# Performance work log

Measured on AMD Instinct MI355X. Metric: run time of the kernel, lower is better.

Reference implementation:

```python
import jax, jax.numpy as jnp
import numpy as np

N_NODES = 40000
N_EDGES = 640000
IN_CH = 128
OUT_CH = 128
BN_EPS = 1e-5


def setup_inputs() -> dict:
    key = jax.random.key(0)
    ks = jax.random.split(key, 8)
    x = jax.random.normal(ks[0], (N_NODES, IN_CH), dtype=jnp.float32)
    edge_index = jax.random.randint(ks[1], (2, N_EDGES), 0, N_NODES, dtype=jnp.int64)
    s1 = 1.0 / np.sqrt(IN_CH)
    s2 = 1.0 / np.sqrt(OUT_CH)
    W1 = jax.random.uniform(ks[2], (OUT_CH, IN_CH), jnp.float32, -s1, s1)
    b1 = jax.random.uniform(ks[3], (OUT_CH,), jnp.float32, -s1, s1)
    gamma = jnp.ones((OUT_CH,), jnp.float32)
    beta = jnp.zeros((OUT_CH,), jnp.float32)
    W2 = jax.random.uniform(ks[4], (OUT_CH, OUT_CH), jnp.float32, -s2, s2)
    b2 = jax.random.uniform(ks[5], (OUT_CH,), jnp.float32, -s2, s2)
    eps = jnp.float32(0.0)
    return {"x": x, "edge_index": edge_index, "W1": W1, "b1": b1,
            "gamma": gamma, "beta": beta, "W2": W2, "b2": b2, "eps": eps}


def reference(x, edge_index, W1, b1, gamma, beta, W2, b2, eps):
    src, dst = edge_index[0], edge_index[1]
    # neighbor sum: agg[v] = sum_{(u,v) in E} x[u]
    agg = jax.ops.segment_sum(x[src], dst, num_segments=N_NODES)  # [N, in_ch]
    h = (1.0 + eps) * x + agg
    # Linear 1
    h = h @ W1.T + b1  # [N, out_ch]
    # BatchNorm1d (training mode: batch stats, biased variance)
    mu = jnp.mean(h, axis=0)
    var = jnp.var(h, axis=0)
    h = (h - mu) * jax.lax.rsqrt(var + BN_EPS) * gamma + beta
    # ReLU + Linear 2
    h = jnp.maximum(h, 0.0)
    return h @ W2.T + b2
```

## Files before the change

### kernel.cpp

```cpp
#include <hip/hip_runtime.h>

#define NN 40000
#define NE 640000
#define BN_EPS 1e-5f

typedef __attribute__((ext_vector_type(8))) short bf16x8;
typedef __attribute__((ext_vector_type(4))) float f32x4;
typedef unsigned int uint;
typedef unsigned short ushort;

__device__ __forceinline__ float blo(uint u) { return __uint_as_float(u << 16); }
__device__ __forceinline__ float bhi(uint u) { return __uint_as_float(u & 0xFFFF0000u); }
__device__ __forceinline__ uint bpack(float lo, float hi) {
    uint a = __float_as_uint(lo); a = (a + 0x7FFFu + ((a >> 16) & 1u)) >> 16;
    uint b = __float_as_uint(hi); b = (b + 0x7FFFu + ((b >> 16) & 1u)) & 0xFFFF0000u;
    return a | b;
}
__device__ __forceinline__ ushort b1pack(float v) {
    uint u = __float_as_uint(v); return (ushort)((u + 0x7FFFu + ((u >> 16) & 1u)) >> 16);
}
__device__ __forceinline__ uint4 cvt8(const float4* f4, int i) {
    float4 p = f4[i * 2], q = f4[i * 2 + 1];
    uint4 o;
    o.x = bpack(p.x, p.y); o.y = bpack(p.z, p.w);
    o.z = bpack(q.x, q.y); o.w = bpack(q.z, q.w);
    return o;
}

__global__ __launch_bounds__(256) void k_pre(const float* __restrict__ x, const float* __restrict__ W1,
                                             const float* __restrict__ W2,
                                             int* __restrict__ cnt, float* __restrict__ bn,
                                             uint* __restrict__ xb, uint* __restrict__ w1b,
                                             uint* __restrict__ w2b) {
    int b = blockIdx.x, t = threadIdx.x;
    if (b < 157) {
        int i = b * 256 + t;
        if (i < NN) cnt[i] = 0;
        if (b == 156) bn[t] = 0.f;
    } else if (b < 2657) {
        int i = (b - 157) * 256 + t;
        ((uint4*)xb)[i] = cvt8((const float4*)x, i);
    } else if (b < 2665) {
        int i = (b - 2657) * 256 + t;
        ((uint4*)w1b)[i] = cvt8((const float4*)W1, i);
    } else {
        int i = (b - 2665) * 256 + t;
        ((uint4*)w2b)[i] = cvt8((const float4*)W2, i);
    }
}

__global__ __launch_bounds__(256) void k_bucket(const int* __restrict__ ei, int* __restrict__ cnt,
                                                ushort* __restrict__ srcl) {
    int e = blockIdx.x * 256 + threadIdx.x;
    if (e >= NE) return;
    int s = ei[e];
    int d = ei[NE + e];
    int pos = atomicAdd(&cnt[d], 1);
    if (pos < 64) srcl[d * 64 + pos] = (ushort)s;
}

__global__ __launch_bounds__(256) void k_gather(const uint* __restrict__ xbv, const int* __restrict__ cnt,
                                                const ushort* __restrict__ srcl, const float* __restrict__ epsp,
                                                uint* __restrict__ hb) {
    int wid = blockIdx.x * 4 + (threadIdx.x >> 6);
    int lane = threadIdx.x & 63;
    int deg = cnt[wid]; deg = deg > 64 ? 64 : deg;
    int sv = srcl[wid * 64 + lane];
    uint su = xbv[wid * 64 + lane];
    float e1 = 1.f + epsp[0];

    uint v[24];
#pragma unroll
    for (int j = 0; j < 24; ++j) {
        int s = __builtin_amdgcn_readlane(sv, j);
        s = (j < deg) ? s : 0;
        v[j] = xbv[(size_t)s * 64 + lane];
    }
    __builtin_amdgcn_sched_barrier(0);

    float p0 = 0.f, p1 = 0.f, p2 = 0.f, p3 = 0.f;
    float r0 = 0.f, r1 = 0.f, r2 = 0.f, r3 = 0.f;
#pragma unroll
    for (int j = 0; j < 24; j += 4) {
        bool k0 = j + 0 < deg, k1 = j + 1 < deg, k2 = j + 2 < deg, k3 = j + 3 < deg;
        p0 += k0 ? blo(v[j + 0]) : 0.f;  r0 += k0 ? bhi(v[j + 0]) : 0.f;
        p1 += k1 ? blo(v[j + 1]) : 0.f;  r1 += k1 ? bhi(v[j + 1]) : 0.f;
        p2 += k2 ? blo(v[j + 2]) : 0.f;  r2 += k2 ? bhi(v[j + 2]) : 0.f;
        p3 += k3 ? blo(v[j + 3]) : 0.f;  r3 += k3 ? bhi(v[j + 3]) : 0.f;
    }
    float a0 = fmaf(blo(su), e1, (p0 + p1) + (p2 + p3));
    float a1 = fmaf(bhi(su), e1, (r0 + r1) + (r2 + r3));

    if (deg > 24) {
        for (int base = 24; base < deg; base += 8) {
#pragma unroll
            for (int j = 0; j < 8; ++j) {
                int idx = base + j;
                int s = __builtin_amdgcn_readlane(sv, idx);
                bool ok = idx < deg;
                s = ok ? s : 0;
                uint vv = xbv[(size_t)s * 64 + lane];
                a0 += ok ? blo(vv) : 0.f;
                a1 += ok ? bhi(vv) : 0.f;
            }
        }
    }
    hb[wid * 64 + lane] = bpack(a0, a1);
}

__global__ __launch_bounds__(256) void k_mm1(const ushort* __restrict__ hb, const ushort* __restrict__ w1b,
                                             const float* __restrict__ b1, ushort* __restrict__ h1b,
                                             float* __restrict__ bnsum, float* __restrict__ bnsumsq) {
    __shared__ float rs[256 * 8];
    __shared__ float rq[256 * 8];
    const int tid = threadIdx.x;
    const int wave = tid >> 6;
    const int lane = tid & 63;
    const int lr = lane & 15;
    const int lk = lane >> 4;
    const int r0 = (blockIdx.x * 4 + wave) * 16;

    bf16x8 a[4];
#pragma unroll
    for (int ks = 0; ks < 4; ++ks)
        a[ks] = *reinterpret_cast<const bf16x8*>(&hb[(size_t)(r0 + lr) * 128 + ks * 32 + lk * 8]);

    f32x4 acc[8];
#pragma unroll
    for (int t = 0; t < 8; ++t) { acc[t][0] = 0.f; acc[t][1] = 0.f; acc[t][2] = 0.f; acc[t][3] = 0.f; }

#pragma unroll
    for (int t = 0; t < 8; ++t) {
        const ushort* wrow = &w1b[(size_t)(t * 16 + lr) * 128];
#pragma unroll
        for (int ks = 0; ks < 4; ++ks) {
            bf16x8 bfr = *reinterpret_cast<const bf16x8*>(&wrow[ks * 32 + lk * 8]);
            acc[t] = __builtin_amdgcn_mfma_f32_16x16x32_bf16(a[ks], bfr, acc[t], 0, 0, 0);
        }
    }
#pragma unroll
    for (int t = 0; t < 8; ++t) {
        float bias = b1[t * 16 + lr];
        float s = 0.f, q = 0.f;
#pragma unroll
        for (int i = 0; i < 4; ++i) {
            float v = acc[t][i] + bias;
            h1b[(size_t)(r0 + lk * 4 + i) * 128 + t * 16 + lr] = b1pack(v);
            s += v; q += v * v;
        }
        rs[tid * 8 + t] = s;
        rq[tid * 8 + t] = q;
    }
    __syncthreads();
    if (tid < 128) {
        int c = tid, t = c >> 4, cr = c & 15;
        float s = 0.f, q = 0.f;
#pragma unroll
        for (int w = 0; w < 4; ++w)
#pragma unroll
            for (int g = 0; g < 4; ++g) {
                int src = w * 64 + g * 16 + cr;
                s += rs[src * 8 + t];
                q += rq[src * 8 + t];
            }
        atomicAdd(&bnsum[c], s);
        atomicAdd(&bnsumsq[c], q);
    }
}

__global__ __launch_bounds__(256) void k_mm2(const ushort* __restrict__ h1b, const ushort* __restrict__ w2b,
                                             const float* __restrict__ b2,
                                             const float* __restrict__ bnsum, const float* __restrict__ bnsumsq,
                                             const float* __restrict__ gamma, const float* __restrict__ beta,
                                             float* __restrict__ out) {
    __shared__ float ssc[128], ssh[128];
    const int tid = threadIdx.x;
    if (tid < 128) {
        float mu = bnsum[tid] * (1.0f / NN);
        float var = bnsumsq[tid] * (1.0f / NN) - mu * mu;
        float rsv = rsqrtf(var + BN_EPS);
        float g = rsv * gamma[tid];
        ssc[tid] = g;
        ssh[tid] = beta[tid] - mu * g;
    }
    __syncthreads();

    const int wave = tid >> 6;
    const int lane = tid & 63;
    const int lr = lane & 15;
    const int lk = lane >> 4;
    const int r0 = (blockIdx.x * 4 + wave) * 16;

    bf16x8 a[4];
#pragma unroll
    for (int ks = 0; ks < 4; ++ks) {
        int kbase = ks * 32 + lk * 8;
        bf16x8 raw = *reinterpret_cast<const bf16x8*>(&h1b[(size_t)(r0 + lr) * 128 + kbase]);
        bf16x8 o;
#pragma unroll
        for (int j = 0; j < 8; ++j) {
            float v = __uint_as_float(((uint)(ushort)raw[j]) << 16);
            v = fmaxf(0.f, fmaf(v, ssc[kbase + j], ssh[kbase + j]));
            o[j] = (short)b1pack(v);
        }
        a[ks] = o;
    }

    f32x4 acc[8];
#pragma unroll
    for (int t = 0; t < 8; ++t) { acc[t][0] = 0.f; acc[t][1] = 0.f; acc[t][2] = 0.f; acc[t][3] = 0.f; }

#pragma unroll
    for (int t = 0; t < 8; ++t) {
        const ushort* wrow = &w2b[(size_t)(t * 16 + lr) * 128];
#pragma unroll
        for (int ks = 0; ks < 4; ++ks) {
            bf16x8 bfr = *reinterpret_cast<const bf16x8*>(&wrow[ks * 32 + lk * 8]);
            acc[t] = __builtin_amdgcn_mfma_f32_16x16x32_bf16(a[ks], bfr, acc[t], 0, 0, 0);
        }
    }
#pragma unroll
    for (int t = 0; t < 8; ++t) {
        float bias = b2[t * 16 + lr];
#pragma unroll
        for (int i = 0; i < 4; ++i)
            out[(size_t)(r0 + lk * 4 + i) * 128 + t * 16 + lr] = acc[t][i] + bias;
    }
}

extern "C" void kernel_launch(void* const* d_in, const int* in_sizes, int n_in,
                              void* d_out, int out_size, void* d_ws, size_t ws_size,
                              hipStream_t stream) {
    const float* x     = (const float*)d_in[0];
    const int*   ei    = (const int*)d_in[1];
    const float* W1    = (const float*)d_in[2];
    const float* b1    = (const float*)d_in[3];
    const float* gamma = (const float*)d_in[4];
    const float* beta  = (const float*)d_in[5];
    const float* W2    = (const float*)d_in[6];
    const float* b2    = (const float*)d_in[7];
    const float* eps   = (const float*)d_in[8];

    char* ws = (char*)d_ws;
    int*    cnt  = (int*)(ws + 0);
    ushort* srcl = (ushort*)(ws + 160000);
    uint*   xb   = (uint*)(ws + 5280000);
    uint*   hb   = (uint*)(ws + 15520000);
    ushort* h1b  = (ushort*)(ws + 25760000);
    uint*   w1b  = (uint*)(ws + 36000000);
    uint*   w2b  = (uint*)(ws + 36032768);
    float*  bn   = (float*)(ws + 36065536);
    float* bnsum   = bn;
    float* bnsumsq = bn + 128;

    k_pre<<<2673, 256, 0, stream>>>(x, W1, W2, cnt, bn, xb, w1b, w2b);
    k_bucket<<<2500, 256, 0, stream>>>(ei, cnt, srcl);
    k_gather<<<10000, 256, 0, stream>>>(xb, cnt, srcl, eps, hb);
    k_mm1<<<625, 256, 0, stream>>>((const ushort*)hb, (const ushort*)w1b, b1, h1b, bnsum, bnsumsq);
    k_mm2<<<625, 256, 0, stream>>>(h1b, (const ushort*)w2b, b2, bnsum, bnsumsq, gamma, beta, (float*)d_out);
}
```

Baseline: 109.3 us.

## Fuse all phases into one cooperative persistent kernel with grid syncs

Replaces the five separate kernel launches with a single cooperative kernel of 512 blocks. It runs conversion plus bucketing, then gather, then mm1, then mm2, with grid.sync between phases and grid-stride loops. The count array is now cleared with a memset, and a multi-kernel path is kept as a fallback if the cooperative launch fails. The aim is to remove launch overhead and inter-kernel gaps, at the cost of grid-wide barriers, a fixed persistent grid that may cut latency hiding in the gather phase, and possible register pressure from launch_bounds(256,2).

```diff
diff --git a/kernel.cpp b/kernel.cpp
--- a/kernel.cpp
+++ b/kernel.cpp
@@ -1,8 +1,13 @@
 #include <hip/hip_runtime.h>
+#include <hip/hip_cooperative_groups.h>
+
+namespace cg = cooperative_groups;
 
 #define NN 40000
 #define NE 640000
 #define BN_EPS 1e-5f
+#define GRID 512
+#define NTHR (GRID * 256)
 
 typedef __attribute__((ext_vector_type(8))) short bf16x8;
 typedef __attribute__((ext_vector_type(4))) float f32x4;
@@ -27,48 +32,37 @@
     return o;
 }
 
-__global__ __launch_bounds__(256) void k_pre(const float* __restrict__ x, const float* __restrict__ W1,
-                                             const float* __restrict__ W2,
-                                             int* __restrict__ cnt, float* __restrict__ bn,
-                                             uint* __restrict__ xb, uint* __restrict__ w1b,
-                                             uint* __restrict__ w2b) {
-    int b = blockIdx.x, t = threadIdx.x;
-    if (b < 157) {
-        int i = b * 256 + t;
-        if (i < NN) cnt[i] = 0;
-        if (b == 156) bn[t] = 0.f;
-    } else if (b < 2657) {
-        int i = (b - 157) * 256 + t;
+
+__device__ __forceinline__ void ph_convert(int gtid, int nthr,
+                                           const float* __restrict__ x, const float* __restrict__ W1,
+                                           const float* __restrict__ W2, uint* __restrict__ xb,
+                                           uint* __restrict__ w1b, uint* __restrict__ w2b,
+                                           float* __restrict__ bn) {
+    if (gtid < 256) bn[gtid] = 0.f;
+    for (int i = gtid; i < 640000; i += nthr)
         ((uint4*)xb)[i] = cvt8((const float4*)x, i);
-    } else if (b < 2665) {
-        int i = (b - 2657) * 256 + t;
+    for (int i = gtid; i < 2048; i += nthr)
         ((uint4*)w1b)[i] = cvt8((const float4*)W1, i);
-    } else {
-        int i = (b - 2665) * 256 + t;
+    for (int i = gtid; i < 2048; i += nthr)
         ((uint4*)w2b)[i] = cvt8((const float4*)W2, i);
-    }
-}
-
-__global__ __launch_bounds__(256) void k_bucket(const int* __restrict__ ei, int* __restrict__ cnt,
-                                                ushort* __restrict__ srcl) {
-    int e = blockIdx.x * 256 + threadIdx.x;
-    if (e >= NE) return;
-    int s = ei[e];
-    int d = ei[NE + e];
-    int pos = atomicAdd(&cnt[d], 1);
-    if (pos < 64) srcl[d * 64 + pos] = (ushort)s;
-}
-
-__global__ __launch_bounds__(256) void k_gather(const uint* __restrict__ xbv, const int* __restrict__ cnt,
-                                                const ushort* __restrict__ srcl, const float* __restrict__ epsp,
-                                                uint* __restrict__ hb) {
-    int wid = blockIdx.x * 4 + (threadIdx.x >> 6);
-    int lane = threadIdx.x & 63;
+}
+
+__device__ __forceinline__ void ph_bucket(int gtid, int nthr, const int* __restrict__ ei,
+                                          int* __restrict__ cnt, ushort* __restrict__ srcl) {
+    for (int e = gtid; e < NE; e += nthr) {
+        int s = ei[e];
+        int d = ei[NE + e];
+        int pos = atomicAdd(&cnt[d], 1);
+        if (pos < 64) srcl[d * 64 + pos] = (ushort)s;
+    }
+}
+
+__device__ __forceinline__ void ph_gather(int wid, int lane, const uint* __restrict__ xbv,
+                                          const int* __restrict__ cnt, const ushort* __restrict__ srcl,
+                                          float e1, uint* __restrict__ hb) {
     int deg = cnt[wid]; deg = deg > 64 ? 64 : deg;
     int sv = srcl[wid * 64 + lane];
     uint su = xbv[wid * 64 + lane];
-    float e1 = 1.f + epsp[0];
-
     uint v[24];
 #pragma unroll
     for (int j = 0; j < 24; ++j) {
@@ -77,20 +71,18 @@
         v[j] = xbv[(size_t)s * 64 + lane];
     }
     __builtin_amdgcn_sched_barrier(0);
-
     float p0 = 0.f, p1 = 0.f, p2 = 0.f, p3 = 0.f;
-    float r0 = 0.f, r1 = 0.f, r2 = 0.f, r3 = 0.f;
+    float q0 = 0.f, q1 = 0.f, q2 = 0.f, q3 = 0.f;
 #pragma unroll
     for (int j = 0; j < 24; j += 4) {
         bool k0 = j + 0 < deg, k1 = j + 1 < deg, k2 = j + 2 < deg, k3 = j + 3 < deg;
-        p0 += k0 ? blo(v[j + 0]) : 0.f;  r0 += k0 ? bhi(v[j + 0]) : 0.f;
-        p1 += k1 ? blo(v[j + 1]) : 0.f;  r1 += k1 ? bhi(v[j + 1]) : 0.f;
-        p2 += k2 ? blo(v[j + 2]) : 0.f;  r2 += k2 ? bhi(v[j + 2]) : 0.f;
-        p3 += k3 ? blo(v[j + 3]) : 0.f;  r3 += k3 ? bhi(v[j + 3]) : 0.f;
+        p0 += k0 ? blo(v[j + 0]) : 0.f;  q0 += k0 ? bhi(v[j + 0]) : 0.f;
+        p1 += k1 ? blo(v[j + 1]) : 0.f;  q1 += k1 ? bhi(v[j + 1]) : 0.f;
+        p2 += k2 ? blo(v[j + 2]) : 0.f;  q2 += k2 ? bhi(v[j + 2]) : 0.f;
+        p3 += k3 ? blo(v[j + 3]) : 0.f;  q3 += k3 ? bhi(v[j + 3]) : 0.f;
     }
     float a0 = fmaf(blo(su), e1, (p0 + p1) + (p2 + p3));
-    float a1 = fmaf(bhi(su), e1, (r0 + r1) + (r2 + r3));
-
+    float a1 = fmaf(bhi(su), e1, (q0 + q1) + (q2 + q3));
     if (deg > 24) {
         for (int base = 24; base < deg; base += 8) {
 #pragma unroll
@@ -108,27 +100,19 @@
     hb[wid * 64 + lane] = bpack(a0, a1);
 }
 
-__global__ __launch_bounds__(256) void k_mm1(const ushort* __restrict__ hb, const ushort* __restrict__ w1b,
-                                             const float* __restrict__ b1, ushort* __restrict__ h1b,
-                                             float* __restrict__ bnsum, float* __restrict__ bnsumsq) {
-    __shared__ float rs[256 * 8];
-    __shared__ float rq[256 * 8];
-    const int tid = threadIdx.x;
-    const int wave = tid >> 6;
-    const int lane = tid & 63;
-    const int lr = lane & 15;
-    const int lk = lane >> 4;
-    const int r0 = (blockIdx.x * 4 + wave) * 16;
-
+__device__ __forceinline__ void ph_mm1(int tile, int tid, float* smem,
+                                       const ushort* __restrict__ hb, const ushort* __restrict__ w1b,
+                                       const float* __restrict__ b1, ushort* __restrict__ h1b,
+                                       float* __restrict__ bnsum, float* __restrict__ bnsumsq) {
+    const int wave = tid >> 6, lane = tid & 63, lr = lane & 15, lk = lane >> 4;
+    const int r0 = tile * 64 + wave * 16;
     bf16x8 a[4];
 #pragma unroll
     for (int ks = 0; ks < 4; ++ks)
         a[ks] = *reinterpret_cast<const bf16x8*>(&hb[(size_t)(r0 + lr) * 128 + ks * 32 + lk * 8]);
-
     f32x4 acc[8];
 #pragma unroll
     for (int t = 0; t < 8; ++t) { acc[t][0] = 0.f; acc[t][1] = 0.f; acc[t][2] = 0.f; acc[t][3] = 0.f; }
-
 #pragma unroll
     for (int t = 0; t < 8; ++t) {
         const ushort* wrow = &w1b[(size_t)(t * 16 + lr) * 128];
@@ -138,15 +122,17 @@
             acc[t] = __builtin_amdgcn_mfma_f32_16x16x32_bf16(a[ks], bfr, acc[t], 0, 0, 0);
         }
     }
+    float* rs = smem;
+    float* rq = smem + 2048;
 #pragma unroll
     for (int t = 0; t < 8; ++t) {
         float bias = b1[t * 16 + lr];
         float s = 0.f, q = 0.f;
 #pragma unroll
         for (int i = 0; i < 4; ++i) {
-            float v = acc[t][i] + bias;
-            h1b[(size_t)(r0 + lk * 4 + i) * 128 + t * 16 + lr] = b1pack(v);
-            s += v; q += v * v;
+            float vv = acc[t][i] + bias;
+            h1b[(size_t)(r0 + lk * 4 + i) * 128 + t * 16 + lr] = b1pack(vv);
+            s += vv; q += vv * vv;
         }
         rs[tid * 8 + t] = s;
         rq[tid * 8 + t] = q;
@@ -166,66 +152,137 @@
         atomicAdd(&bnsum[c], s);
         atomicAdd(&bnsumsq[c], q);
     }
-}
-
-__global__ __launch_bounds__(256) void k_mm2(const ushort* __restrict__ h1b, const ushort* __restrict__ w2b,
-                                             const float* __restrict__ b2,
-                                             const float* __restrict__ bnsum, const float* __restrict__ bnsumsq,
-                                             const float* __restrict__ gamma, const float* __restrict__ beta,
-                                             float* __restrict__ out) {
+    __syncthreads();
+}
+
+__device__ __forceinline__ void ph_mm2(int tile, int tid, const float* ssc, const float* ssh,
+                                       const ushort* __restrict__ h1b, const ushort* __restrict__ w2b,
+                                       const float* __restrict__ b2, float* __restrict__ out) {
+    const int wave = tid >> 6, lane = tid & 63, lr = lane & 15, lk = lane >> 4;
+    const int r0 = tile * 64 + wave * 16;
+    bf16x8 a[4];
+#pragma unroll
+    for (int ks = 0; ks < 4; ++ks) {
+        int kbase = ks * 32 + lk * 8;
+        bf16x8 raw = *reinterpret_cast<const bf16x8*>(&h1b[(size_t)(r0 + lr) * 128 + kbase]);
+        bf16x8 o;
+#pragma unroll
+        for (int j = 0; j < 8; ++j) {
+            float vv = __uint_as_float(((uint)(ushort)raw[j]) << 16);
+            vv = fmaxf(0.f, fmaf(vv, ssc[kbase + j], ssh[kbase + j]));
+            o[j] = (short)b1pack(vv);
+        }
+        a[ks] = o;
+    }
+    f32x4 acc[8];
+#pragma unroll
+    for (int t = 0; t < 8; ++t) { acc[t][0] = 0.f; acc[t][1] = 0.f; acc[t][2] = 0.f; acc[t][3] = 0.f; }
+#pragma unroll
+    for (int t = 0; t < 8; ++t) {
+        const ushort* wrow = &w2b[(size_t)(t * 16 + lr) * 128];
+#pragma unroll
+        for (int ks = 0; ks < 4; ++ks) {
+            bf16x8 bfr = *reinterpret_cast<const bf16x8*>(&wrow[ks * 32 + lk * 8]);
+            acc[t] = __builtin_amdgcn_mfma_f32_16x16x32_bf16(a[ks], bfr, acc[t], 0, 0, 0);
+        }
+    }
+#pragma unroll
+    for (int t = 0; t < 8; ++t) {
+        float bias = b2[t * 16 + lr];
+#pragma unroll
+        for (int i = 0; i < 4; ++i)
+            out[(size_t)(r0 + lk * 4 + i) * 128 + t * 16 + lr] = acc[t][i] + bias;
+    }
+}
+
+__global__ __launch_bounds__(256, 2) void k_fused(
+        const float* __restrict__ x, const int* __restrict__ ei,
+        const float* __restrict__ W1, const float* __restrict__ b1,
+        const float* __restrict__ gamma, const float* __restrict__ beta,
+        const float* __restrict__ W2, const float* __restrict__ b2,
+        const float* __restrict__ epsp,
+        int* __restrict__ cnt, ushort* __restrict__ srcl, uint* __restrict__ xb,
+        uint* __restrict__ hb, ushort* __restrict__ h1b,
+        uint* __restrict__ w1b, uint* __restrict__ w2b,
+        float* __restrict__ bn, float* __restrict__ out) {
+    cg::grid_group grid = cg::this_grid();
+    __shared__ float smem[4096];
+    const int tid = threadIdx.x;
+    const int bid = blockIdx.x;
+    const int gtid = bid * 256 + tid;
+
+    ph_convert(gtid, NTHR, x, W1, W2, xb, w1b, w2b, bn);
+    ph_bucket(gtid, NTHR, ei, cnt, srcl);
+    grid.sync();
+
+    {
+        const float e1 = 1.f + epsp[0];
+        const int gwave = bid * 4 + (tid >> 6);
+        const int lane = tid & 63;
+        for (int wid = gwave; wid < NN; wid += GRID * 4)
+            ph_gather(wid, lane, xb, cnt, srcl, e1, hb);
+    }
+    grid.sync();
+
+    for (int tile = bid; tile < 625; tile += GRID)
+        ph_mm1(tile, tid, smem, (const ushort*)hb, (const ushort*)w1b, b1, h1b, bn, bn + 128);
+    grid.sync();
+
+    {
+        float* ssc = smem;
+        float* ssh = smem + 128;
+        if (tid < 128) {
+            float mu = bn[tid] * (1.0f / NN);
+            float var = bn[128 + tid] * (1.0f / NN) - mu * mu;
+            float rsv = rsqrtf(var + BN_EPS);
+            float g = rsv * gamma[tid];
+            ssc[tid] = g;
+            ssh[tid] = beta[tid] - mu * g;
+        }
+        __syncthreads();
+        for (int tile = bid; tile < 625; tile += GRID)
+            ph_mm2(tile, tid, ssc, ssh, h1b, (const ushort*)w2b, b2, out);
+    }
+}
+
+__global__ __launch_bounds__(256) void k_pre_f(const float* __restrict__ x, const float* __restrict__ W1,
+                                               const float* __restrict__ W2, uint* __restrict__ xb,
+                                               uint* __restrict__ w1b, uint* __restrict__ w2b,
+                                               float* __restrict__ bn) {
+    ph_convert(blockIdx.x * 256 + threadIdx.x, 2560 * 256, x, W1, W2, xb, w1b, w2b, bn);
+}
+__global__ __launch_bounds__(256) void k_bucket_f(const int* __restrict__ ei, int* __restrict__ cnt,
+                                                  ushort* __restrict__ srcl) {
+    ph_bucket(blockIdx.x * 256 + threadIdx.x, 2500 * 256, ei, cnt, srcl);
+}
+__global__ __launch_bounds__(256) void k_gather_f(const uint* __restrict__ xb, const int* __restrict__ cnt,
+                                                  const ushort* __restrict__ srcl,
+                                                  const float* __restrict__ epsp, uint* __restrict__ hb) {
+    int wid = blockIdx.x * 4 + (threadIdx.x >> 6);
+    ph_gather(wid, threadIdx.x & 63, xb, cnt, srcl, 1.f + epsp[0], hb);
+}
+__global__ __launch_bounds__(256) void k_mm1_f(const ushort* __restrict__ hb, const ushort* __restrict__ w1b,
+                                               const float* __restrict__ b1, ushort* __restrict__ h1b,
+                                               float* __restrict__ bn) {
+    __shared__ float smem[4096];
+    ph_mm1(blockIdx.x, threadIdx.x, smem, hb, w1b, b1, h1b, bn, bn + 128);
+}
+__global__ __launch_bounds__(256) void k_mm2_f(const ushort* __restrict__ h1b, const ushort* __restrict__ w2b,
+                                               const float* __restrict__ b2, const float* __restrict__ bn,
+                                               const float* __restrict__ gamma, const float* __restrict__ beta,
+                                               float* __restrict__ out) {
     __shared__ float ssc[128], ssh[128];
-    const int tid = threadIdx.x;
+    int tid = threadIdx.x;
     if (tid < 128) {
-        float mu = bnsum[tid] * (1.0f / NN);
-        float var = bnsumsq[tid] * (1.0f / NN) - mu * mu;
+        float mu = bn[tid] * (1.0f / NN);
+        float var = bn[128 + tid] * (1.0f / NN) - mu * mu;
         float rsv = rsqrtf(var + BN_EPS);
         float g = rsv * gamma[tid];
         ssc[tid] = g;
         ssh[tid] = beta[tid] - mu * g;
     }
     __syncthreads();
-
-    const int wave = tid >> 6;
-    const int lane = tid & 63;
-    const int lr = lane & 15;
-    const int lk = lane >> 4;
-    const int r0 = (blockIdx.x * 4 + wave) * 16;
-
-    bf16x8 a[4];
-#pragma unroll
-    for (int ks = 0; ks < 4; ++ks) {
-        int kbase = ks * 32 + lk * 8;
-        bf16x8 raw = *reinterpret_cast<const bf16x8*>(&h1b[(size_t)(r0 + lr) * 128 + kbase]);
-        bf16x8 o;
-#pragma unroll
-        for (int j = 0; j < 8; ++j) {
-            float v = __uint_as_float(((uint)(ushort)raw[j]) << 16);
-            v = fmaxf(0.f, fmaf(v, ssc[kbase + j], ssh[kbase + j]));
-            o[j] = (short)b1pack(v);
-        }
-        a[ks] = o;
-    }
-
-    f32x4 acc[8];
-#pragma unroll
-    for (int t = 0; t < 8; ++t) { acc[t][0] = 0.f; acc[t][1] = 0.f; acc[t][2] = 0.f; acc[t][3] = 0.f; }
-
-#pragma unroll
-    for (int t = 0; t < 8; ++t) {
-        const ushort* wrow = &w2b[(size_t)(t * 16 + lr) * 128];
-#pragma unroll
-        for (int ks = 0; ks < 4; ++ks) {
-            bf16x8 bfr = *reinterpret_cast<const bf16x8*>(&wrow[ks * 32 + lk * 8]);
-            acc[t] = __builtin_amdgcn_mfma_f32_16x16x32_bf16(a[ks], bfr, acc[t], 0, 0, 0);
-        }
-    }
-#pragma unroll
-    for (int t = 0; t < 8; ++t) {
-        float bias = b2[t * 16 + lr];
-#pragma unroll
-        for (int i = 0; i < 4; ++i)
-            out[(size_t)(r0 + lk * 4 + i) * 128 + t * 16 + lr] = acc[t][i] + bias;
-    }
+    ph_mm2(blockIdx.x, tid, ssc, ssh, h1b, w2b, b2, out);
 }
 
 extern "C" void kernel_launch(void* const* d_in, const int* in_sizes, int n_in,
@@ -250,12 +307,19 @@
     uint*   w1b  = (uint*)(ws + 36000000);
     uint*   w2b  = (uint*)(ws + 36032768);
     float*  bn   = (float*)(ws + 36065536);
-    float* bnsum   = bn;
-    float* bnsumsq = bn + 128;
-
-    k_pre<<<2673, 256, 0, stream>>>(x, W1, W2, cnt, bn, xb, w1b, w2b);
-    k_bucket<<<2500, 256, 0, stream>>>(ei, cnt, srcl);
-    k_gather<<<10000, 256, 0, stream>>>(xb, cnt, srcl, eps, hb);
-    k_mm1<<<625, 256, 0, stream>>>((const ushort*)hb, (const ushort*)w1b, b1, h1b, bnsum, bnsumsq);
-    k_mm2<<<625, 256, 0, stream>>>(h1b, (const ushort*)w2b, b2, bnsum, bnsumsq, gamma, beta, (float*)d_out);
-}
+    float*  outp = (float*)d_out;
+
+    hipMemsetAsync(cnt, 0, 160000, stream);
+
+    void* kargs[] = { (void*)&x, (void*)&ei, (void*)&W1, (void*)&b1, (void*)&gamma, (void*)&beta,
+                      (void*)&W2, (void*)&b2, (void*)&eps, (void*)&cnt, (void*)&srcl, (void*)&xb,
+                      (void*)&hb, (void*)&h1b, (void*)&w1b, (void*)&w2b, (void*)&bn, (void*)&outp };
+    hipError_t err = hipLaunchCooperativeKernel(k_fused, dim3(GRID), dim3(256), kargs, 0u, stream);
+    if (err != hipSuccess) {
+        k_pre_f<<<2560, 256, 0, stream>>>(x, W1, W2, xb, w1b, w2b, bn);
+        k_bucket_f<<<2500, 256, 0, stream>>>(ei, cnt, srcl);
+        k_gather_f<<<10000, 256, 0, stream>>>(xb, cnt, srcl, eps, hb);
+        k_mm1_f<<<625, 256, 0, stream>>>((const ushort*)hb, (const ushort*)w1b, b1, h1b, bn);
+        k_mm2_f<<<625, 256, 0, stream>>>(h1b, (const ushort*)w2b, b2, bn, gamma, beta, outp);
+    }
+}
```

Result: slower. 308.6 us (+182.3%).
